# Kernel optimization log

Measured on AMD Instinct MI355X. Metric: run time of the kernel, lower is better.

## Reference

```python
import jax, jax.numpy as jnp
import numpy as np

DIM = 512
DIM_HEAD = 64
HEADS = 8
DIM_INNER = DIM_HEAD * HEADS
EPS = float(jnp.finfo(jnp.float32).eps)  # torch nn.RMSNorm default eps


def setup_inputs() -> dict:
    key = jax.random.key(0)
    k1, k2, k3, k4 = jax.random.split(key, 4)
    tokens = jax.random.normal(k1, (2, 4096, DIM), dtype=jnp.float32)
    norm_weight = jnp.ones((DIM,), dtype=jnp.float32)
    s = 1.0 / np.sqrt(DIM)
    w_qkv = jax.random.normal(k2, (DIM, 3 * DIM_INNER), dtype=jnp.float32) * s
    w_out = jax.random.normal(k3, (DIM_INNER, DIM), dtype=jnp.float32) * (1.0 / np.sqrt(DIM_INNER))
    return {"tokens": tokens, "norm_weight": norm_weight, "w_qkv": w_qkv, "w_out": w_out}


def reference(tokens, norm_weight, w_qkv, w_out):
    b, n, d = tokens.shape
    scale = DIM_HEAD ** -0.5
    # RMSNorm
    ms = jnp.mean(jnp.square(tokens), axis=-1, keepdims=True)
    x = tokens * jax.lax.rsqrt(ms + EPS) * norm_weight
    # QKV projection, split heads: b n (qkv h d) -> qkv b h n d
    qkv = x @ w_qkv                                   # [b, n, 3*h*dh]
    qkv = qkv.reshape(b, n, 3, HEADS, DIM_HEAD)
    q, k, v = jnp.moveaxis(qkv, 2, 0)                 # each [b, n, h, dh]
    q = jnp.swapaxes(q, 1, 2)                         # [b, h, n, dh]
    k = jnp.swapaxes(k, 1, 2)
    v = jnp.swapaxes(v, 1, 2)
    # naive attention (note: original applies no scale in forward, self.scale unused)
    sim = jnp.einsum('bhid,bhjd->bhij', q, k)
    attn = jax.nn.softmax(sim, axis=-1)
    out = jnp.einsum('bhij,bhjd->bhid', attn, v)
    out = jnp.swapaxes(out, 1, 2).reshape(b, n, DIM_INNER)
    return out @ w_out
```

## Files before the change

kernel.cpp:

```cpp
#include <hip/hip_runtime.h>
#include <stdint.h>
#include <stddef.h>

typedef _Float16 half_t;
typedef __attribute__((ext_vector_type(2))) __fp16 fp16v2;
typedef __attribute__((ext_vector_type(4))) _Float16 f16x4;
typedef __attribute__((ext_vector_type(8))) _Float16 f16x8;
typedef __attribute__((ext_vector_type(4))) float f32x4;

#define EPSF 1.1920928955078125e-07f
#define LOG2E 1.4426950408889634f

#define AS1 __attribute__((address_space(1)))
#define AS3 __attribute__((address_space(3)))

#define WS_XN   0u
#define WS_WQT  4194304u
#define WS_WOT  4980736u
#define WS_Q    5242880u
#define WS_K    9437184u
#define WS_VT   13631488u
#define WS_AO   17825792u
#define WS_NEED_BYTES 44040192u

__device__ __forceinline__ void gload16(const void* g, void* l) {
  __builtin_amdgcn_global_load_lds((const AS1 void*)g, (AS3 void*)l, 16, 0, 0);
}

__device__ __forceinline__ float fast_exp2(float x) {
#if __has_builtin(__builtin_amdgcn_exp2f)
  return __builtin_amdgcn_exp2f(x);
#else
  return exp2f(x);
#endif
}

__global__ __launch_bounds__(256) void k_rmsnorm(const float* __restrict__ t,
                                                 const float* __restrict__ w,
                                                 half_t* __restrict__ xn) {
  int row = blockIdx.x * 4 + (threadIdx.x >> 6);
  int ln = threadIdx.x & 63;
  const float* src = t + (size_t)row * 512 + ln * 8;
  float4 a = *(const float4*)src;
  float4 b = *(const float4*)(src + 4);
  float ss = a.x * a.x + a.y * a.y + a.z * a.z + a.w * a.w
           + b.x * b.x + b.y * b.y + b.z * b.z + b.w * b.w;
#pragma unroll
  for (int m = 32; m >= 1; m >>= 1) ss += __shfl_xor(ss, m);
  float r = rsqrtf(ss * (1.0f / 512.0f) + EPSF);
  const float* wp = w + ln * 8;
  float4 w0 = *(const float4*)wp;
  float4 w1 = *(const float4*)(wp + 4);
  f16x8 o;
  o[0] = (_Float16)(a.x * r * w0.x);
  o[1] = (_Float16)(a.y * r * w0.y);
  o[2] = (_Float16)(a.z * r * w0.z);
  o[3] = (_Float16)(a.w * r * w0.w);
  o[4] = (_Float16)(b.x * r * w1.x);
  o[5] = (_Float16)(b.y * r * w1.y);
  o[6] = (_Float16)(b.z * r * w1.z);
  o[7] = (_Float16)(b.w * r * w1.w);
  *(f16x8*)(xn + (size_t)row * 512 + ln * 8) = o;
}

__global__ __launch_bounds__(256) void k_wtrans(const float* __restrict__ wqkv,
                                                const float* __restrict__ wout,
                                                half_t* __restrict__ wqt,
                                                half_t* __restrict__ wot) {
  __shared__ half_t tile[64][65];
  int b = blockIdx.x;
  const float* src; half_t* dst; int N, tk, tn;
  if (b < 192) { src = wqkv; dst = wqt; N = 1536; tk = b / 24; tn = b - tk * 24; }
  else { b -= 192; src = wout; dst = wot; N = 512; tk = b >> 3; tn = b & 7; }
  int c = threadIdx.x & 63;
  int r0 = threadIdx.x >> 6;
#pragma unroll
  for (int i = 0; i < 16; ++i) {
    int r = i * 4 + r0;
    tile[r][c] = (_Float16)src[(size_t)(tk * 64 + r) * N + tn * 64 + c];
  }
  __syncthreads();
#pragma unroll
  for (int i = 0; i < 16; ++i) {
    int n = i * 4 + r0;
    dst[(size_t)(tn * 64 + n) * 512 + tk * 64 + c] = tile[c][n];
  }
}

__device__ __forceinline__ void gemm_core(const half_t* __restrict__ A,
                                          const half_t* __restrict__ Bt,
                                          int m0, int n0, int Ksz,
                                          half_t* Al, half_t* Bl,
                                          f32x4 acc[4][4]) {
  int wv = threadIdx.x >> 6, ln = threadIdx.x & 63;
  int wm = (wv >> 1) << 6, wn = (wv & 1) << 6;
  for (int kt = 0; kt < Ksz; kt += 64) {
#pragma unroll
    for (int i = 0; i < 4; ++i) {
      int seg = wv * 4 + i;
      int r = seg * 8 + (ln >> 3);
      int cb = ((ln & 7) * 16) ^ ((r & 7) << 4);
      gload16((const char*)(A + (size_t)(m0 + r) * Ksz + kt) + cb, (char*)Al + seg * 1024);
      gload16((const char*)(Bt + (size_t)(n0 + r) * Ksz + kt) + cb, (char*)Bl + seg * 1024);
    }
    __syncthreads();
#pragma unroll
    for (int kc = 0; kc < 2; ++kc) {
      f16x8 af[4], bf[4];
#pragma unroll
      for (int mt = 0; mt < 4; ++mt) {
        int rr = wm + mt * 16 + (ln & 15);
        af[mt] = *(const f16x8*)((const char*)Al + rr * 128 +
                                 ((kc * 64 + (ln >> 4) * 16) ^ ((rr & 7) << 4)));
      }
#pragma unroll
      for (int nt = 0; nt < 4; ++nt) {
        int rr = wn + nt * 16 + (ln & 15);
        bf[nt] = *(const f16x8*)((const char*)Bl + rr * 128 +
                                 ((kc * 64 + (ln >> 4) * 16) ^ ((rr & 7) << 4)));
      }
#pragma unroll
      for (int mt = 0; mt < 4; ++mt)
#pragma unroll
        for (int nt = 0; nt < 4; ++nt)
          acc[mt][nt] = __builtin_amdgcn_mfma_f32_16x16x32_f16(af[mt], bf[nt], acc[mt][nt], 0, 0, 0);
    }
    __syncthreads();
  }
}

__global__ __launch_bounds__(256, 2) void k_gemm_qkv(const half_t* __restrict__ A,
                                                     const half_t* __restrict__ Bt,
                                                     half_t* __restrict__ q,
                                                     half_t* __restrict__ kk,
                                                     half_t* __restrict__ vt) {
  __shared__ __align__(16) half_t Al[128 * 64];
  __shared__ __align__(16) half_t Bl[128 * 64];
  f32x4 acc[4][4];
  f32x4 z = {0.f, 0.f, 0.f, 0.f};
#pragma unroll
  for (int i = 0; i < 4; ++i)
#pragma unroll
    for (int j = 0; j < 4; ++j) acc[i][j] = z;
  int m0 = blockIdx.x * 128, n0 = blockIdx.y * 128;
  gemm_core(A, Bt, m0, n0, 512, Al, Bl, acc);
  int wv = threadIdx.x >> 6, ln = threadIdx.x & 63;
  int wm = (wv >> 1) << 6, wn = (wv & 1) << 6;
#pragma unroll
  for (int mt = 0; mt < 4; ++mt) {
#pragma unroll
    for (int nt = 0; nt < 4; ++nt) {
      int gn = n0 + wn + nt * 16 + (ln & 15);
      int qkv_i = gn >> 9;
      int h = (gn >> 6) & 7;
      int d = gn & 63;
#pragma unroll
      for (int j = 0; j < 4; ++j) {
        int gm = m0 + wm + mt * 16 + (ln >> 4) * 4 + j;
        int head = ((gm >> 12) << 3) | h;
        int n = gm & 4095;
        float av = acc[mt][nt][j];
        if (qkv_i == 0)      q [((size_t)head * 4096 + n) * 64 + d] = (_Float16)(av * LOG2E);
        else if (qkv_i == 1) kk[((size_t)head * 4096 + n) * 64 + d] = (_Float16)av;
        else {
          int pcol = (n & ~31) | (((n >> 2) & 3) << 3) | (((n >> 4) & 1) << 2) | (n & 3);
          vt[((size_t)head * 64 + d) * 4096 + pcol] = (_Float16)av;
        }
      }
    }
  }
}

__global__ __launch_bounds__(256, 2) void k_gemm_out(const half_t* __restrict__ A,
                                                     const half_t* __restrict__ Bt,
                                                     float* __restrict__ out) {
  __shared__ __align__(16) half_t Al[128 * 64];
  __shared__ __align__(16) half_t Bl[128 * 64];
  f32x4 acc[4][4];
  f32x4 z = {0.f, 0.f, 0.f, 0.f};
#pragma unroll
  for (int i = 0; i < 4; ++i)
#pragma unroll
    for (int j = 0; j < 4; ++j) acc[i][j] = z;
  int m0 = blockIdx.x * 128, n0 = blockIdx.y * 128;
  gemm_core(A, Bt, m0, n0, 512, Al, Bl, acc);
  int wv = threadIdx.x >> 6, ln = threadIdx.x & 63;
  int wm = (wv >> 1) << 6, wn = (wv & 1) << 6;
#pragma unroll
  for (int mt = 0; mt < 4; ++mt)
#pragma unroll
    for (int nt = 0; nt < 4; ++nt) {
      int gn = n0 + wn + nt * 16 + (ln & 15);
#pragma unroll
      for (int j = 0; j < 4; ++j) {
        int gm = m0 + wm + mt * 16 + (ln >> 4) * 4 + j;
        out[(size_t)gm * 512 + gn] = acc[mt][nt][j];
      }
    }
}

__global__ __launch_bounds__(512, 4) void k_attn(const half_t* __restrict__ q,
                                                 const half_t* __restrict__ kg,
                                                 const half_t* __restrict__ vt,
                                                 half_t* __restrict__ ao) {
  __shared__ __align__(16) char lds[32768];
  const int wv = threadIdx.x >> 6, ln = threadIdx.x & 63;
  const int bid = blockIdx.x;
  const int lin = (bid & 7) * 64 + (bid >> 3);
  const int head = lin >> 5;
  const int qt = lin & 31;
  const int q0 = qt * 128 + wv * 16;
  const char* qh = (const char*)(q  + (size_t)head * 4096 * 64);
  const char* kh = (const char*)(kg + (size_t)head * 4096 * 64);
  const char* vh = (const char*)(vt + (size_t)head * 64 * 4096);

  f16x8 qf[2];
#pragma unroll
  for (int kc = 0; kc < 2; ++kc) {
    int r = q0 + (ln & 15);
    qf[kc] = *(const f16x8*)(qh + (size_t)r * 128 + kc * 64 + (ln >> 4) * 16);
  }

  const int sr = wv * 8 + (ln >> 3);
  const int cb = ((ln & 7) * 16) ^ ((sr & 7) << 4);
  const char* ks = kh + (size_t)sr * 128 + cb;
  const char* vs = vh + (size_t)sr * 8192 + cb;
  const int lo = wv * 1024;

  float mrun = -1e30f;
  f32x4 oacc[4];
  f32x4 lacc;
  const f32x4 z = {0.f, 0.f, 0.f, 0.f};
  lacc = z;
#pragma unroll
  for (int dt = 0; dt < 4; ++dt) oacc[dt] = z;
  f16x8 ones;
#pragma unroll
  for (int e = 0; e < 8; ++e) ones[e] = (_Float16)1.0f;

  gload16(ks, lds + lo);
  gload16(vs, lds + 8192 + lo);
  ks += 8192; vs += 128;
  __syncthreads();

  int cur = 0;
#pragma unroll 1
  for (int t = 0; t < 64; ++t) {
    if (t < 63) {
      char* base = lds + (cur ^ 1) * 16384;
      gload16(ks, base + lo);
      gload16(vs, base + 8192 + lo);
      ks += 8192; vs += 128;
    }
    const char* Kb = lds + cur * 16384;
    const char* Vb = Kb + 8192;

    f32x4 s[4];
#pragma unroll
    for (int kt = 0; kt < 4; ++kt) s[kt] = z;
    __builtin_amdgcn_s_setprio(1);
#pragma unroll
    for (int kc = 0; kc < 2; ++kc) {
      f16x8 kf[4];
#pragma unroll
      for (int kt = 0; kt < 4; ++kt) {
        int rr = kt * 16 + (ln & 15);
        kf[kt] = *(const f16x8*)(Kb + rr * 128 + ((kc * 64 + (ln >> 4) * 16) ^ ((rr & 7) << 4)));
      }
#pragma unroll
      for (int kt = 0; kt < 4; ++kt)
        s[kt] = __builtin_amdgcn_mfma_f32_16x16x32_f16(kf[kt], qf[kc], s[kt], 0, 0, 0);
    }
    __builtin_amdgcn_s_setprio(0);

    f16x8 vf[2][4];
#pragma unroll
    for (int dt = 0; dt < 4; ++dt) {
      int rr = dt * 16 + (ln & 15);
      int sw = (rr & 7) << 4;
      vf[0][dt] = *(const f16x8*)(Vb + rr * 128 + (((ln >> 4) * 16) ^ sw));
      vf[1][dt] = *(const f16x8*)(Vb + rr * 128 + ((64 + (ln >> 4) * 16) ^ sw));
    }

    f16x8 pf[2];
    {
      float a0 = fmaxf(fmaxf(s[0][0], s[0][1]), fmaxf(s[0][2], s[0][3]));
      float a1 = fmaxf(fmaxf(s[1][0], s[1][1]), fmaxf(s[1][2], s[1][3]));
      float a2 = fmaxf(fmaxf(s[2][0], s[2][1]), fmaxf(s[2][2], s[2][3]));
      float a3 = fmaxf(fmaxf(s[3][0], s[3][1]), fmaxf(s[3][2], s[3][3]));
      float tm = fmaxf(fmaxf(a0, a1), fmaxf(a2, a3));
      tm = fmaxf(tm, __shfl_xor(tm, 16));
      tm = fmaxf(tm, __shfl_xor(tm, 32));
      if (__any(tm > mrun + 11.0f)) {
        float mnew = fmaxf(mrun, tm);
        float sc = fast_exp2(mrun - mnew);
        mrun = mnew;
        lacc[0] *= sc;
#pragma unroll
        for (int dt = 0; dt < 4; ++dt) {
          oacc[dt][0] *= sc; oacc[dt][1] *= sc;
          oacc[dt][2] *= sc; oacc[dt][3] *= sc;
        }
      }
      float p[4][4];
#pragma unroll
      for (int kt = 0; kt < 4; ++kt)
#pragma unroll
        for (int r = 0; r < 4; ++r) p[kt][r] = fast_exp2(s[kt][r] - mrun);
#pragma unroll
      for (int kc = 0; kc < 2; ++kc) {
        union { f16x8 v; fp16v2 h[4]; } u;
        u.h[0] = __builtin_amdgcn_cvt_pkrtz(p[2 * kc][0], p[2 * kc][1]);
        u.h[1] = __builtin_amdgcn_cvt_pkrtz(p[2 * kc][2], p[2 * kc][3]);
        u.h[2] = __builtin_amdgcn_cvt_pkrtz(p[2 * kc + 1][0], p[2 * kc + 1][1]);
        u.h[3] = __builtin_amdgcn_cvt_pkrtz(p[2 * kc + 1][2], p[2 * kc + 1][3]);
        pf[kc] = u.v;
      }
    }

    __builtin_amdgcn_s_setprio(1);
#pragma unroll
    for (int dt = 0; dt < 4; ++dt)
      oacc[dt] = __builtin_amdgcn_mfma_f32_16x16x32_f16(vf[0][dt], pf[0], oacc[dt], 0, 0, 0);
    lacc = __builtin_amdgcn_mfma_f32_16x16x32_f16(ones, pf[0], lacc, 0, 0, 0);
#pragma unroll
    for (int dt = 0; dt < 4; ++dt)
      oacc[dt] = __builtin_amdgcn_mfma_f32_16x16x32_f16(vf[1][dt], pf[1], oacc[dt], 0, 0, 0);
    lacc = __builtin_amdgcn_mfma_f32_16x16x32_f16(ones, pf[1], lacc, 0, 0, 0);
    __builtin_amdgcn_s_setprio(0);

    __syncthreads();
    cur ^= 1;
  }

  const int b = head >> 3, h = head & 7;
  {
    float inv = 1.0f / lacc[0];
    int n = q0 + (ln & 15);
    half_t* dst = ao + ((size_t)(b * 4096 + n)) * 512 + h * 64 + (ln >> 4) * 4;
#pragma unroll
    for (int dt = 0; dt < 4; ++dt) {
      f16x4 o4;
      o4[0] = (_Float16)(oacc[dt][0] * inv);
      o4[1] = (_Float16)(oacc[dt][1] * inv);
      o4[2] = (_Float16)(oacc[dt][2] * inv);
      o4[3] = (_Float16)(oacc[dt][3] * inv);
      *(f16x4*)(dst + dt * 16) = o4;
    }
  }
}

extern "C" void kernel_launch(void* const* d_in, const int* in_sizes, int n_in,
                              void* d_out, int out_size, void* d_ws, size_t ws_size,
                              hipStream_t stream) {
  if (ws_size < WS_NEED_BYTES) return;
  const float* tokens = (const float*)d_in[0];
  const float* nw     = (const float*)d_in[1];
  const float* wqkv   = (const float*)d_in[2];
  const float* wout   = (const float*)d_in[3];
  float* out = (float*)d_out;
  half_t* ws = (half_t*)d_ws;
  half_t* xn  = ws + WS_XN;
  half_t* wqt = ws + WS_WQT;
  half_t* wot = ws + WS_WOT;
  half_t* qb  = ws + WS_Q;
  half_t* kb  = ws + WS_K;
  half_t* vtb = ws + WS_VT;
  half_t* aob = ws + WS_AO;

  k_rmsnorm<<<2048, 256, 0, stream>>>(tokens, nw, xn);
  k_wtrans<<<256, 256, 0, stream>>>(wqkv, wout, wqt, wot);
  k_gemm_qkv<<<dim3(64, 12), 256, 0, stream>>>(xn, wqt, qb, kb, vtb);
  k_attn<<<512, 512, 0, stream>>>(qb, kb, vtb, aob);
  k_gemm_out<<<dim3(64, 4), 256, 0, stream>>>(aob, wot, out);
}
```

Before: 135.4 us.

## Double KV tile size per barrier and fold running max into MFMA accumulator init

The attention kernel now stages 128 keys per double-buffered stage (64KB LDS) and processes them as two 64-key subtiles between barriers, halving syncthreads and prefetch issue count. It precomputes swizzled LDS addresses, unrolls the ping-pong loop via macros, and initializes the score accumulator with -mrun so the subtraction is folded into the MFMA. The rescale check skips the cross-lane max reduction in the common case. Doubling LDS per block may reduce occupancy (launch bounds ask for 4 blocks of 512 threads).

```diff
diff --git a/kernel.cpp b/kernel.cpp
--- a/kernel.cpp
+++ b/kernel.cpp
@@ -203,7 +203,7 @@
                                                  const half_t* __restrict__ kg,
                                                  const half_t* __restrict__ vt,
                                                  half_t* __restrict__ ao) {
-  __shared__ __align__(16) char lds[32768];
+  __shared__ __align__(16) char lds[65536];
   const int wv = threadIdx.x >> 6, ln = threadIdx.x & 63;
   const int bid = blockIdx.x;
   const int lin = (bid & 7) * 64 + (bid >> 3);
@@ -221,13 +221,23 @@
     qf[kc] = *(const f16x8*)(qh + (size_t)r * 128 + kc * 64 + (ln >> 4) * 16);
   }
 
-  const int sr = wv * 8 + (ln >> 3);
-  const int cb = ((ln & 7) * 16) ^ ((sr & 7) << 4);
-  const char* ks = kh + (size_t)sr * 128 + cb;
-  const char* vs = vh + (size_t)sr * 8192 + cb;
-  const int lo = wv * 1024;
-
-  float mrun = -1e30f;
+  const int la0 = (ln & 15) * 128 + (((ln >> 4) * 16) ^ ((ln & 7) << 4));
+  const int la1 = (ln & 15) * 128 + ((64 + (ln >> 4) * 16) ^ ((ln & 7) << 4));
+
+  const char* ks0; const char* ks1; const char* vs0; const char* vs1;
+  int loK0, loK1, loV0, loV1;
+  {
+    int i0 = wv * 2, i1 = wv * 2 + 1;
+    int cb = ((ln & 7) * 16) ^ (((ln >> 3) & 7) << 4);
+    int rK0 = i0 * 8 + (ln >> 3), rK1 = i1 * 8 + (ln >> 3);
+    ks0 = kh + (size_t)rK0 * 128 + cb;  loK0 = i0 * 1024;
+    ks1 = kh + (size_t)rK1 * 128 + cb;  loK1 = i1 * 1024;
+    int rV0 = (i0 & 7) * 8 + (ln >> 3), rV1 = (i1 & 7) * 8 + (ln >> 3);
+    vs0 = vh + (size_t)rV0 * 8192 + (i0 >> 3) * 128 + cb;  loV0 = 16384 + i0 * 1024;
+    vs1 = vh + (size_t)rV1 * 8192 + (i1 >> 3) * 128 + cb;  loV1 = 16384 + i1 * 1024;
+  }
+
+  float mrun = 0.0f;
   f32x4 oacc[4];
   f32x4 lacc;
   const f32x4 z = {0.f, 0.f, 0.f, 0.f};
@@ -238,100 +248,102 @@
 #pragma unroll
   for (int e = 0; e < 8; ++e) ones[e] = (_Float16)1.0f;
 
-  gload16(ks, lds + lo);
-  gload16(vs, lds + 8192 + lo);
-  ks += 8192; vs += 128;
+  gload16(ks0, lds + loK0); gload16(ks1, lds + loK1);
+  gload16(vs0, lds + loV0); gload16(vs1, lds + loV1);
+  ks0 += 16384; ks1 += 16384; vs0 += 256; vs1 += 256;
   __syncthreads();
 
-  int cur = 0;
+#define SUBTILE(KOFF, VOFF) do {                                               \
+    f32x4 s[4];                                                                \
+    { float nm = -mrun; f32x4 mi = {nm, nm, nm, nm};                           \
+      s[0] = mi; s[1] = mi; s[2] = mi; s[3] = mi; }                            \
+    __builtin_amdgcn_s_setprio(1);                                             \
+    {                                                                          \
+      f16x8 kf0[4], kf1[4];                                                    \
+      _Pragma("unroll") for (int kt = 0; kt < 4; ++kt)                         \
+        kf0[kt] = *(const f16x8*)(lds + (KOFF) + kt * 2048 + la0);             \
+      _Pragma("unroll") for (int kt = 0; kt < 4; ++kt)                         \
+        s[kt] = __builtin_amdgcn_mfma_f32_16x16x32_f16(kf0[kt], qf[0], s[kt], 0, 0, 0); \
+      _Pragma("unroll") for (int kt = 0; kt < 4; ++kt)                         \
+        kf1[kt] = *(const f16x8*)(lds + (KOFF) + kt * 2048 + la1);             \
+      _Pragma("unroll") for (int kt = 0; kt < 4; ++kt)                         \
+        s[kt] = __builtin_amdgcn_mfma_f32_16x16x32_f16(kf1[kt], qf[1], s[kt], 0, 0, 0); \
+    }                                                                          \
+    __builtin_amdgcn_s_setprio(0);                                             \
+    f16x8 vf[2][4];                                                            \
+    _Pragma("unroll") for (int dt = 0; dt < 4; ++dt) {                         \
+      vf[0][dt] = *(const f16x8*)(lds + (VOFF) + dt * 2048 + la0);             \
+      vf[1][dt] = *(const f16x8*)(lds + (VOFF) + dt * 2048 + la1);             \
+    }                                                                          \
+    f16x8 pf[2];                                                               \
+    {                                                                          \
+      float m0_ = fmaxf(fmaxf(s[0][0], s[0][1]), s[0][2]);                     \
+      float m1_ = fmaxf(fmaxf(s[0][3], s[1][0]), s[1][1]);                     \
+      float m2_ = fmaxf(fmaxf(s[1][2], s[1][3]), s[2][0]);                     \
+      float m3_ = fmaxf(fmaxf(s[2][1], s[2][2]), s[2][3]);                     \
+      float m4_ = fmaxf(fmaxf(s[3][0], s[3][1]), s[3][2]);                     \
+      float m5_ = fmaxf(fmaxf(m0_, m1_), m2_);                                 \
+      float tm = fmaxf(fmaxf(fmaxf(m3_, m4_), s[3][3]), m5_);                  \
+      float p[4][4];                                                           \
+      if (__builtin_expect(__any(tm > 11.0f), 0)) {          \
+        tm = fmaxf(tm, __shfl_xor(tm, 16));                                    \
+        tm = fmaxf(tm, __shfl_xor(tm, 32));                                    \
+        float dlt = fmaxf(tm, 0.0f);                                           \
+        float sc = fast_exp2(-dlt);                                            \
+        mrun += dlt;                                                           \
+        lacc[0] *= sc;                                                         \
+        _Pragma("unroll") for (int dt = 0; dt < 4; ++dt) {                     \
+          oacc[dt][0] *= sc; oacc[dt][1] *= sc;                                \
+          oacc[dt][2] *= sc; oacc[dt][3] *= sc;                                \
+        }                                                                      \
+        _Pragma("unroll") for (int kt = 0; kt < 4; ++kt)                       \
+          _Pragma("unroll") for (int r = 0; r < 4; ++r)                        \
+            p[kt][r] = fast_exp2(s[kt][r] - dlt);                              \
+      } else {                                                                 \
+        _Pragma("unroll") for (int kt = 0; kt < 4; ++kt)                       \
+          _Pragma("unroll") for (int r = 0; r < 4; ++r)                        \
+            p[kt][r] = fast_exp2(s[kt][r]);                                    \
+      }                                                                        \
+      _Pragma("unroll") for (int kc = 0; kc < 2; ++kc) {                       \
+        union { f16x8 v; fp16v2 h[4]; } u;                                     \
+        u.h[0] = __builtin_amdgcn_cvt_pkrtz(p[2 * kc][0], p[2 * kc][1]);       \
+        u.h[1] = __builtin_amdgcn_cvt_pkrtz(p[2 * kc][2], p[2 * kc][3]);       \
+        u.h[2] = __builtin_amdgcn_cvt_pkrtz(p[2 * kc + 1][0], p[2 * kc + 1][1]); \
+        u.h[3] = __builtin_amdgcn_cvt_pkrtz(p[2 * kc + 1][2], p[2 * kc + 1][3]); \
+        pf[kc] = u.v;                                                          \
+      }                                                                        \
+    }                                                                          \
+    __builtin_amdgcn_s_setprio(1);                                             \
+    _Pragma("unroll") for (int dt = 0; dt < 4; ++dt)                           \
+      oacc[dt] = __builtin_amdgcn_mfma_f32_16x16x32_f16(vf[0][dt], pf[0], oacc[dt], 0, 0, 0); \
+    lacc = __builtin_amdgcn_mfma_f32_16x16x32_f16(ones, pf[0], lacc, 0, 0, 0); \
+    _Pragma("unroll") for (int dt = 0; dt < 4; ++dt)                           \
+      oacc[dt] = __builtin_amdgcn_mfma_f32_16x16x32_f16(vf[1][dt], pf[1], oacc[dt], 0, 0, 0); \
+    lacc = __builtin_amdgcn_mfma_f32_16x16x32_f16(ones, pf[1], lacc, 0, 0, 0); \
+    __builtin_amdgcn_s_setprio(0);                                             \
+  } while (0)
+
+#define BIGTILE(CUROFF, NXTOFF, PREFETCH) do {                                 \
+    if (PREFETCH) {                                                            \
+      gload16(ks0, lds + (NXTOFF) + loK0); gload16(ks1, lds + (NXTOFF) + loK1);\
+      gload16(vs0, lds + (NXTOFF) + loV0); gload16(vs1, lds + (NXTOFF) + loV1);\
+      ks0 += 16384; ks1 += 16384; vs0 += 256; vs1 += 256;                      \
+    }                                                                          \
+    SUBTILE((CUROFF), (CUROFF) + 16384);                                       \
+    SUBTILE((CUROFF) + 8192, (CUROFF) + 24576);                                \
+    __syncthreads();                                                           \
+  } while (0)
+
 #pragma unroll 1
-  for (int t = 0; t < 64; ++t) {
-    if (t < 63) {
-      char* base = lds + (cur ^ 1) * 16384;
-      gload16(ks, base + lo);
-      gload16(vs, base + 8192 + lo);
-      ks += 8192; vs += 128;
-    }
-    const char* Kb = lds + cur * 16384;
-    const char* Vb = Kb + 8192;
-
-    f32x4 s[4];
-#pragma unroll
-    for (int kt = 0; kt < 4; ++kt) s[kt] = z;
-    __builtin_amdgcn_s_setprio(1);
-#pragma unroll
-    for (int kc = 0; kc < 2; ++kc) {
-      f16x8 kf[4];
-#pragma unroll
-      for (int kt = 0; kt < 4; ++kt) {
-        int rr = kt * 16 + (ln & 15);
-        kf[kt] = *(const f16x8*)(Kb + rr * 128 + ((kc * 64 + (ln >> 4) * 16) ^ ((rr & 7) << 4)));
-      }
-#pragma unroll
-      for (int kt = 0; kt < 4; ++kt)
-        s[kt] = __builtin_amdgcn_mfma_f32_16x16x32_f16(kf[kt], qf[kc], s[kt], 0, 0, 0);
-    }
-    __builtin_amdgcn_s_setprio(0);
-
-    f16x8 vf[2][4];
-#pragma unroll
-    for (int dt = 0; dt < 4; ++dt) {
-      int rr = dt * 16 + (ln & 15);
-      int sw = (rr & 7) << 4;
-      vf[0][dt] = *(const f16x8*)(Vb + rr * 128 + (((ln >> 4) * 16) ^ sw));
-      vf[1][dt] = *(const f16x8*)(Vb + rr * 128 + ((64 + (ln >> 4) * 16) ^ sw));
-    }
-
-    f16x8 pf[2];
-    {
-      float a0 = fmaxf(fmaxf(s[0][0], s[0][1]), fmaxf(s[0][2], s[0][3]));
-      float a1 = fmaxf(fmaxf(s[1][0], s[1][1]), fmaxf(s[1][2], s[1][3]));
-      float a2 = fmaxf(fmaxf(s[2][0], s[2][1]), fmaxf(s[2][2], s[2][3]));
-      float a3 = fmaxf(fmaxf(s[3][0], s[3][1]), fmaxf(s[3][2], s[3][3]));
-      float tm = fmaxf(fmaxf(a0, a1), fmaxf(a2, a3));
-      tm = fmaxf(tm, __shfl_xor(tm, 16));
-      tm = fmaxf(tm, __shfl_xor(tm, 32));
-      if (__any(tm > mrun + 11.0f)) {
-        float mnew = fmaxf(mrun, tm);
-        float sc = fast_exp2(mrun - mnew);
-        mrun = mnew;
-        lacc[0] *= sc;
-#pragma unroll
-        for (int dt = 0; dt < 4; ++dt) {
-          oacc[dt][0] *= sc; oacc[dt][1] *= sc;
-          oacc[dt][2] *= sc; oacc[dt][3] *= sc;
-        }
-      }
-      float p[4][4];
-#pragma unroll
-      for (int kt = 0; kt < 4; ++kt)
-#pragma unroll
-        for (int r = 0; r < 4; ++r) p[kt][r] = fast_exp2(s[kt][r] - mrun);
-#pragma unroll
-      for (int kc = 0; kc < 2; ++kc) {
-        union { f16x8 v; fp16v2 h[4]; } u;
-        u.h[0] = __builtin_amdgcn_cvt_pkrtz(p[2 * kc][0], p[2 * kc][1]);
-        u.h[1] = __builtin_amdgcn_cvt_pkrtz(p[2 * kc][2], p[2 * kc][3]);
-        u.h[2] = __builtin_amdgcn_cvt_pkrtz(p[2 * kc + 1][0], p[2 * kc + 1][1]);
-        u.h[3] = __builtin_amdgcn_cvt_pkrtz(p[2 * kc + 1][2], p[2 * kc + 1][3]);
-        pf[kc] = u.v;
-      }
-    }
-
-    __builtin_amdgcn_s_setprio(1);
-#pragma unroll
-    for (int dt = 0; dt < 4; ++dt)
-      oacc[dt] = __builtin_amdgcn_mfma_f32_16x16x32_f16(vf[0][dt], pf[0], oacc[dt], 0, 0, 0);
-    lacc = __builtin_amdgcn_mfma_f32_16x16x32_f16(ones, pf[0], lacc, 0, 0, 0);
-#pragma unroll
-    for (int dt = 0; dt < 4; ++dt)
-      oacc[dt] = __builtin_amdgcn_mfma_f32_16x16x32_f16(vf[1][dt], pf[1], oacc[dt], 0, 0, 0);
-    lacc = __builtin_amdgcn_mfma_f32_16x16x32_f16(ones, pf[1], lacc, 0, 0, 0);
-    __builtin_amdgcn_s_setprio(0);
-
-    __syncthreads();
-    cur ^= 1;
-  }
+  for (int t = 0; t < 30; t += 2) {
+    BIGTILE(0, 32768, 1);
+    BIGTILE(32768, 0, 1);
+  }
+  BIGTILE(0, 32768, 1);
+  BIGTILE(32768, 0, 0);
+
+#undef BIGTILE
+#undef SUBTILE
 
   const int b = head >> 3, h = head & 7;
   {
```

After: 151.0 us. 11.5% more time.

## Software-pipeline attention loop so PV MFMAs overlap next tile's QK

Applied to the files above, without the earlier changes.

Restructures the flash-attention inner loop into a software pipeline. The PV MFMAs for the previous tile now issue right after the QK MFMAs of the current tile, so matrix work can overlap the softmax VALU and LDS reads, with a prologue and epilogue added. It also folds the running max into the QK accumulator init (-mrun), so the exp needs no per-element subtraction, and starts mrun at 0 with a rescale only when the tile max exceeds 11. This adds register pressure, since V fragments and P are carried across iterations.

```diff
diff --git a/kernel.cpp b/kernel.cpp
--- a/kernel.cpp
+++ b/kernel.cpp
@@ -227,7 +227,7 @@
   const char* vs = vh + (size_t)sr * 8192 + cb;
   const int lo = wv * 1024;
 
-  float mrun = -1e30f;
+  float mrun = 0.0f;
   f32x4 oacc[4];
   f32x4 lacc;
   const f32x4 z = {0.f, 0.f, 0.f, 0.f};
@@ -238,100 +238,121 @@
 #pragma unroll
   for (int e = 0; e < 8; ++e) ones[e] = (_Float16)1.0f;
 
+  f16x8 vfp0[4], vfp1[4];
+  f16x8 pfp[2];
+  f32x4 s[4];
+
+#define QK(KB) do {                                                            \
+    float nm = -mrun;                                                          \
+    f32x4 mi = {nm, nm, nm, nm};                                               \
+    s[0] = mi; s[1] = mi; s[2] = mi; s[3] = mi;                                \
+    _Pragma("unroll") for (int kc = 0; kc < 2; ++kc) {                         \
+      f16x8 kf[4];                                                             \
+      _Pragma("unroll") for (int kt = 0; kt < 4; ++kt) {                       \
+        int rr = kt * 16 + (ln & 15);                                          \
+        kf[kt] = *(const f16x8*)((KB) + rr * 128 +                             \
+                 ((kc * 64 + (ln >> 4) * 16) ^ ((rr & 7) << 4)));              \
+      }                                                                        \
+      _Pragma("unroll") for (int kt = 0; kt < 4; ++kt)                         \
+        s[kt] = __builtin_amdgcn_mfma_f32_16x16x32_f16(kf[kt], qf[kc], s[kt], 0, 0, 0); \
+    }                                                                          \
+  } while (0)
+
+#define PV() do {                                                              \
+    _Pragma("unroll") for (int dt = 0; dt < 4; ++dt)                           \
+      oacc[dt] = __builtin_amdgcn_mfma_f32_16x16x32_f16(vfp0[dt], pfp[0], oacc[dt], 0, 0, 0); \
+    lacc = __builtin_amdgcn_mfma_f32_16x16x32_f16(ones, pfp[0], lacc, 0, 0, 0); \
+    _Pragma("unroll") for (int dt = 0; dt < 4; ++dt)                           \
+      oacc[dt] = __builtin_amdgcn_mfma_f32_16x16x32_f16(vfp1[dt], pfp[1], oacc[dt], 0, 0, 0); \
+    lacc = __builtin_amdgcn_mfma_f32_16x16x32_f16(ones, pfp[1], lacc, 0, 0, 0); \
+  } while (0)
+
+#define VLOAD(VB) do {                                                         \
+    _Pragma("unroll") for (int dt = 0; dt < 4; ++dt) {                         \
+      int rr = dt * 16 + (ln & 15);                                            \
+      int sw = (rr & 7) << 4;                                                  \
+      vfp0[dt] = *(const f16x8*)((VB) + rr * 128 + (((ln >> 4) * 16) ^ sw));   \
+      vfp1[dt] = *(const f16x8*)((VB) + rr * 128 + ((64 + (ln >> 4) * 16) ^ sw)); \
+    }                                                                          \
+  } while (0)
+
+#define SMPACK() do {                                                          \
+    float m0_ = fmaxf(fmaxf(s[0][0], s[0][1]), s[0][2]);                       \
+    float m1_ = fmaxf(fmaxf(s[0][3], s[1][0]), s[1][1]);                       \
+    float m2_ = fmaxf(fmaxf(s[1][2], s[1][3]), s[2][0]);                       \
+    float m3_ = fmaxf(fmaxf(s[2][1], s[2][2]), s[2][3]);                       \
+    float m4_ = fmaxf(fmaxf(s[3][0], s[3][1]), s[3][2]);                       \
+    float m5_ = fmaxf(fmaxf(m0_, m1_), m2_);                                   \
+    float tm = fmaxf(fmaxf(fmaxf(m3_, m4_), s[3][3]), m5_);                    \
+    tm = fmaxf(tm, __shfl_xor(tm, 16));                                        \
+    tm = fmaxf(tm, __shfl_xor(tm, 32));                                        \
+    if (__builtin_expect(__any(tm > 11.0f), 0)) {       \
+      float dlt = fmaxf(tm, 0.0f);                                             \
+      float sc = fast_exp2(-dlt);                                              \
+      mrun += dlt;                                                             \
+      lacc[0] *= sc;                                                           \
+      _Pragma("unroll") for (int dt = 0; dt < 4; ++dt) {                       \
+        oacc[dt][0] *= sc; oacc[dt][1] *= sc;                                  \
+        oacc[dt][2] *= sc; oacc[dt][3] *= sc;                                  \
+      }                                                                        \
+      _Pragma("unroll") for (int kt = 0; kt < 4; ++kt)                         \
+        _Pragma("unroll") for (int r = 0; r < 4; ++r)                          \
+          s[kt][r] = fast_exp2(s[kt][r] - dlt);                                \
+    } else {                                                                   \
+      _Pragma("unroll") for (int kt = 0; kt < 4; ++kt)                         \
+        _Pragma("unroll") for (int r = 0; r < 4; ++r)                          \
+          s[kt][r] = fast_exp2(s[kt][r]);                                      \
+    }                                                                          \
+    _Pragma("unroll") for (int kc = 0; kc < 2; ++kc) {                         \
+      union { f16x8 v; fp16v2 h[4]; } u;                                       \
+      u.h[0] = __builtin_amdgcn_cvt_pkrtz(s[2 * kc][0], s[2 * kc][1]);         \
+      u.h[1] = __builtin_amdgcn_cvt_pkrtz(s[2 * kc][2], s[2 * kc][3]);         \
+      u.h[2] = __builtin_amdgcn_cvt_pkrtz(s[2 * kc + 1][0], s[2 * kc + 1][1]); \
+      u.h[3] = __builtin_amdgcn_cvt_pkrtz(s[2 * kc + 1][2], s[2 * kc + 1][3]); \
+      pfp[kc] = u.v;                                                           \
+    }                                                                          \
+  } while (0)
+
   gload16(ks, lds + lo);
   gload16(vs, lds + 8192 + lo);
   ks += 8192; vs += 128;
   __syncthreads();
 
-  int cur = 0;
+  {
+    gload16(ks, lds + 16384 + lo);
+    gload16(vs, lds + 16384 + 8192 + lo);
+    ks += 8192; vs += 128;
+    __builtin_amdgcn_s_setprio(1);
+    QK(lds);
+    __builtin_amdgcn_s_setprio(0);
+    VLOAD(lds + 8192);
+    SMPACK();
+    __syncthreads();
+  }
+
 #pragma unroll 1
-  for (int t = 0; t < 64; ++t) {
+  for (int t = 1; t < 64; ++t) {
     if (t < 63) {
-      char* base = lds + (cur ^ 1) * 16384;
+      char* base = lds + ((t + 1) & 1) * 16384;
       gload16(ks, base + lo);
       gload16(vs, base + 8192 + lo);
       ks += 8192; vs += 128;
     }
-    const char* Kb = lds + cur * 16384;
-    const char* Vb = Kb + 8192;
-
-    f32x4 s[4];
-#pragma unroll
-    for (int kt = 0; kt < 4; ++kt) s[kt] = z;
+    const char* Kb = lds + (t & 1) * 16384;
     __builtin_amdgcn_s_setprio(1);
-#pragma unroll
-    for (int kc = 0; kc < 2; ++kc) {
-      f16x8 kf[4];
-#pragma unroll
-      for (int kt = 0; kt < 4; ++kt) {
-        int rr = kt * 16 + (ln & 15);
-        kf[kt] = *(const f16x8*)(Kb + rr * 128 + ((kc * 64 + (ln >> 4) * 16) ^ ((rr & 7) << 4)));
-      }
-#pragma unroll
-      for (int kt = 0; kt < 4; ++kt)
-        s[kt] = __builtin_amdgcn_mfma_f32_16x16x32_f16(kf[kt], qf[kc], s[kt], 0, 0, 0);
-    }
+    QK(Kb);
+    PV();
     __builtin_amdgcn_s_setprio(0);
-
-    f16x8 vf[2][4];
-#pragma unroll
-    for (int dt = 0; dt < 4; ++dt) {
-      int rr = dt * 16 + (ln & 15);
-      int sw = (rr & 7) << 4;
-      vf[0][dt] = *(const f16x8*)(Vb + rr * 128 + (((ln >> 4) * 16) ^ sw));
-      vf[1][dt] = *(const f16x8*)(Vb + rr * 128 + ((64 + (ln >> 4) * 16) ^ sw));
-    }
-
-    f16x8 pf[2];
-    {
-      float a0 = fmaxf(fmaxf(s[0][0], s[0][1]), fmaxf(s[0][2], s[0][3]));
-      float a1 = fmaxf(fmaxf(s[1][0], s[1][1]), fmaxf(s[1][2], s[1][3]));
-      float a2 = fmaxf(fmaxf(s[2][0], s[2][1]), fmaxf(s[2][2], s[2][3]));
-      float a3 = fmaxf(fmaxf(s[3][0], s[3][1]), fmaxf(s[3][2], s[3][3]));
-      float tm = fmaxf(fmaxf(a0, a1), fmaxf(a2, a3));
-      tm = fmaxf(tm, __shfl_xor(tm, 16));
-      tm = fmaxf(tm, __shfl_xor(tm, 32));
-      if (__any(tm > mrun + 11.0f)) {
-        float mnew = fmaxf(mrun, tm);
-        float sc = fast_exp2(mrun - mnew);
-        mrun = mnew;
-        lacc[0] *= sc;
-#pragma unroll
-        for (int dt = 0; dt < 4; ++dt) {
-          oacc[dt][0] *= sc; oacc[dt][1] *= sc;
-          oacc[dt][2] *= sc; oacc[dt][3] *= sc;
-        }
-      }
-      float p[4][4];
-#pragma unroll
-      for (int kt = 0; kt < 4; ++kt)
-#pragma unroll
-        for (int r = 0; r < 4; ++r) p[kt][r] = fast_exp2(s[kt][r] - mrun);
-#pragma unroll
-      for (int kc = 0; kc < 2; ++kc) {
-        union { f16x8 v; fp16v2 h[4]; } u;
-        u.h[0] = __builtin_amdgcn_cvt_pkrtz(p[2 * kc][0], p[2 * kc][1]);
-        u.h[1] = __builtin_amdgcn_cvt_pkrtz(p[2 * kc][2], p[2 * kc][3]);
-        u.h[2] = __builtin_amdgcn_cvt_pkrtz(p[2 * kc + 1][0], p[2 * kc + 1][1]);
-        u.h[3] = __builtin_amdgcn_cvt_pkrtz(p[2 * kc + 1][2], p[2 * kc + 1][3]);
-        pf[kc] = u.v;
-      }
-    }
-
-    __builtin_amdgcn_s_setprio(1);
-#pragma unroll
-    for (int dt = 0; dt < 4; ++dt)
-      oacc[dt] = __builtin_amdgcn_mfma_f32_16x16x32_f16(vf[0][dt], pf[0], oacc[dt], 0, 0, 0);
-    lacc = __builtin_amdgcn_mfma_f32_16x16x32_f16(ones, pf[0], lacc, 0, 0, 0);
-#pragma unroll
-    for (int dt = 0; dt < 4; ++dt)
-      oacc[dt] = __builtin_amdgcn_mfma_f32_16x16x32_f16(vf[1][dt], pf[1], oacc[dt], 0, 0, 0);
-    lacc = __builtin_amdgcn_mfma_f32_16x16x32_f16(ones, pf[1], lacc, 0, 0, 0);
-    __builtin_amdgcn_s_setprio(0);
-
+    VLOAD(Kb + 8192);
+    SMPACK();
     __syncthreads();
-    cur ^= 1;
-  }
+  }
+  PV();
+
+#undef QK
+#undef PV
+#undef VLOAD
+#undef SMPACK
 
   const int b = head >> 3, h = head & 7;
   {
```

Result: no change. 135.4 us (-0.0%).
